# Kernel tuning notes

Measured on AMD Instinct MI355X. Metric: run time of the kernel, lower is better.

The kernel has to match this reference:

```python
import jax, jax.numpy as jnp
import numpy as np

N_NODES = 100000
N_EDGES = 1600000
D_IN = 256
N_HEADS = 4
D_OUT = 32
NEG_SLOPE = 0.2


def setup_inputs() -> dict:
    key = jax.random.key(0)
    k1, k2, k3, k4, k5, k6 = jax.random.split(key, 6)
    x = jax.random.normal(k1, (N_NODES, D_IN), dtype=jnp.float32)
    fc_w = jax.random.normal(k2, (N_HEADS * D_OUT, D_IN), dtype=jnp.float32) * (1.0 / np.sqrt(D_IN))
    attn_l = jax.random.normal(k3, (N_HEADS, D_OUT), dtype=jnp.float32) * 0.1
    attn_r = jax.random.normal(k4, (N_HEADS, D_OUT), dtype=jnp.float32) * 0.1
    src = jax.random.randint(k5, (N_EDGES,), 0, N_NODES, dtype=jnp.int64)
    dst = jax.random.randint(k6, (N_EDGES,), 0, N_NODES, dtype=jnp.int64)
    return {"x": x, "fc_w": fc_w, "attn_l": attn_l, "attn_r": attn_r, "src": src, "dst": dst}


def reference(x, fc_w, attn_l, attn_r, src, dst):
    N = x.shape[0]
    H, F = attn_l.shape
    # Linear projection: ft = fc(x) viewed as [N, H, F]
    ft = (x @ fc_w.T).reshape(N, H, F)
    # Per-node attention logits: el = <ft, a_l>, er = <ft, a_r>  -> [N, H]
    el = jnp.einsum("nhf,hf->nh", ft, attn_l)
    er = jnp.einsum("nhf,hf->nh", ft, attn_r)
    # Edge scores: e = leaky_relu(el[src] + er[dst])  -> [E, H]
    e = el[src] + er[dst]
    e = jnp.where(e > 0, e, NEG_SLOPE * e)
    # Segment (per-destination-node) softmax over incoming edges
    m = jax.ops.segment_max(e, dst, num_segments=N)  # [N, H]
    ex = jnp.exp(e - m[dst])                          # [E, H]
    denom = jax.ops.segment_sum(ex, dst, num_segments=N)  # [N, H]
    a = ex / denom[dst]                               # [E, H]
    # Weighted scatter-sum aggregation: out[n] = sum_{e: dst=n} a_e * ft[src_e]
    out = jax.ops.segment_sum(ft[src] * a[:, :, None], dst, num_segments=N)  # [N, H, F]
    return out
```

## Files before the change

### kernel.cpp

```cpp
#include <hip/hip_runtime.h>
#include <math.h>

#define N_NODES 100000
#define N_EDGES 1600000
#define D_IN 256
#define N_HEADS 4
#define D_OUT 32
#define D_HID 128
#define NEG_SLOPE 0.2f

#define BUCKET_SHIFT 8
#define BUCKET_NODES 256
#define NB ((N_NODES + BUCKET_NODES - 1) / BUCKET_NODES)
#define CAP 6144
#define TILE 8192
#define N_TILES ((N_EDGES + TILE - 1) / TILE)

typedef __attribute__((ext_vector_type(8))) short bf16x8;
typedef __attribute__((ext_vector_type(4))) float f32x4;

static __device__ __forceinline__ unsigned short f2bf(float f) {
  union { float f; unsigned u; } c; c.f = f;
  unsigned r = c.u + 0x7FFFu + ((c.u >> 16) & 1u);
  return (unsigned short)(r >> 16);
}
static __device__ __forceinline__ float bfu_lo(unsigned u) {
  union { unsigned u; float f; } c; c.u = u << 16; return c.f;
}
static __device__ __forceinline__ float bfu_hi(unsigned u) {
  union { unsigned u; float f; } c; c.u = u & 0xFFFF0000u; return c.f;
}

#define LDA 40
__global__ __launch_bounds__(256) void k_gemm(const float* __restrict__ x,
                                              const float* __restrict__ w,
                                              unsigned short* __restrict__ ftb) {
  __shared__ short As[128 * LDA];
  __shared__ short Bs[128 * LDA];
  int t = threadIdx.x;
  int wave = t >> 6, lane = t & 63;
  int quad = lane >> 4, l16 = lane & 15;
  int rowBase = blockIdx.x * 128;
  int wm = (wave >> 1) * 64, wn = (wave & 1) * 64;
  f32x4 acc[4][4];
  #pragma unroll
  for (int mt = 0; mt < 4; ++mt)
    #pragma unroll
    for (int nt = 0; nt < 4; ++nt) {
      acc[mt][nt][0] = 0.f; acc[mt][nt][1] = 0.f;
      acc[mt][nt][2] = 0.f; acc[mt][nt][3] = 0.f;
    }

  for (int kb = 0; kb < D_IN; kb += 32) {
    #pragma unroll
    for (int p = 0; p < 4; ++p) {
      int idx = p * 256 + t;
      int r = idx >> 3;
      int kq = (idx & 7) * 4;
      int row = rowBase + r;
      float4 v = make_float4(0.f, 0.f, 0.f, 0.f);
      if (row < N_NODES) v = *(const float4*)&x[(size_t)row * D_IN + kb + kq];
      short* d = &As[r * LDA + kq];
      d[0] = (short)f2bf(v.x); d[1] = (short)f2bf(v.y);
      d[2] = (short)f2bf(v.z); d[3] = (short)f2bf(v.w);
    }
    #pragma unroll
    for (int p = 0; p < 4; ++p) {
      int idx = p * 256 + t;
      int r = idx >> 3;
      int kq = (idx & 7) * 4;
      float4 v = *(const float4*)&w[(size_t)r * D_IN + kb + kq];
      short* d = &Bs[r * LDA + kq];
      d[0] = (short)f2bf(v.x); d[1] = (short)f2bf(v.y);
      d[2] = (short)f2bf(v.z); d[3] = (short)f2bf(v.w);
    }
    __syncthreads();
    bf16x8 af[4], bfr[4];
    #pragma unroll
    for (int mt = 0; mt < 4; ++mt)
      af[mt] = *(const bf16x8*)&As[(wm + mt * 16 + l16) * LDA + quad * 8];
    #pragma unroll
    for (int nt = 0; nt < 4; ++nt)
      bfr[nt] = *(const bf16x8*)&Bs[(wn + nt * 16 + l16) * LDA + quad * 8];
    #pragma unroll
    for (int mt = 0; mt < 4; ++mt)
      #pragma unroll
      for (int nt = 0; nt < 4; ++nt)
        acc[mt][nt] = __builtin_amdgcn_mfma_f32_16x16x32_bf16(af[mt], bfr[nt], acc[mt][nt], 0, 0, 0);
    __syncthreads();
  }
  #pragma unroll
  for (int mt = 0; mt < 4; ++mt) {
    #pragma unroll
    for (int nt = 0; nt < 4; ++nt) {
      int col = wn + nt * 16 + l16;
      #pragma unroll
      for (int r = 0; r < 4; ++r) {
        int row = rowBase + wm + mt * 16 + quad * 4 + r;
        if (row < N_NODES)
          ftb[(size_t)row * D_HID + col] = f2bf(acc[mt][nt][r]);
      }
    }
  }
}

__global__ void k_eler(const unsigned short* __restrict__ ftb,
                       const float* __restrict__ al,
                       const float* __restrict__ ar,
                       float* __restrict__ el, float* __restrict__ er) {
  int gid = blockIdx.x * blockDim.x + threadIdx.x;
  if (gid >= N_NODES * N_HEADS) return;
  int n = gid >> 2, h = gid & 3;
  const unsigned* f = (const unsigned*)&ftb[(size_t)n * D_HID + h * D_OUT];
  const float* alh = &al[h * D_OUT];
  const float* arh = &ar[h * D_OUT];
  float sl = 0.f, sr = 0.f;
  #pragma unroll
  for (int i = 0; i < 16; ++i) {
    unsigned u = f[i];
    float lo = bfu_lo(u), hi = bfu_hi(u);
    sl += lo * alh[2 * i] + hi * alh[2 * i + 1];
    sr += lo * arh[2 * i] + hi * arh[2 * i + 1];
  }
  el[gid] = sl;
  er[gid] = sr;
}

__global__ __launch_bounds__(256) void k_bucket(const int* __restrict__ src,
                                                const int* __restrict__ dst,
                                                int* __restrict__ gfill,
                                                unsigned* __restrict__ pairs) {
  __shared__ int bcnt[NB];
  __shared__ int brsv[NB];
  __shared__ int brank[NB];
  int t = threadIdx.x;
  for (int tile = blockIdx.x; tile < N_TILES; tile += gridDim.x) {
    int e0 = tile * TILE;
    int e1 = min(e0 + TILE, N_EDGES);
    for (int i = t; i < NB; i += 256) { bcnt[i] = 0; brank[i] = 0; }
    __syncthreads();
    for (int i = e0 + t; i < e1; i += 256)
      atomicAdd(&bcnt[dst[i] >> BUCKET_SHIFT], 1);
    __syncthreads();
    for (int i = t; i < NB; i += 256) {
      int c = bcnt[i];
      brsv[i] = (c > 0) ? atomicAdd(&gfill[i], c) : 0;
    }
    __syncthreads();
    for (int i = e0 + t; i < e1; i += 256) {
      int d = dst[i];
      int s = src[i];
      int b = d >> BUCKET_SHIFT;
      int r = brsv[b] + atomicAdd(&brank[b], 1);
      if (r < CAP)
        pairs[(size_t)b * CAP + r] = ((unsigned)s << 8) | (unsigned)(d & (BUCKET_NODES - 1));
    }
    __syncthreads();
  }
}

__global__ __launch_bounds__(512) void k_scanbuckets(const int* __restrict__ gfill,
                                                     int* __restrict__ bbase,
                                                     int* __restrict__ offs) {
  __shared__ int ss[512];
  int t = threadIdx.x;
  int v = (t < NB) ? gfill[t] : 0;
  ss[t] = v;
  __syncthreads();
  #pragma unroll
  for (int d = 1; d < 512; d <<= 1) {
    int u = (t >= d) ? ss[t - d] : 0;
    __syncthreads();
    ss[t] += u;
    __syncthreads();
  }
  if (t < NB) bbase[t] = (t == 0) ? 0 : ss[t - 1];
  if (t == 0) offs[N_NODES] = N_EDGES;
}

__global__ __launch_bounds__(256) void k_localsort(const unsigned* __restrict__ pairs,
                                                   const int* __restrict__ gfill,
                                                   const int* __restrict__ bbase,
                                                   int* __restrict__ offs,
                                                   int* __restrict__ ssrc) {
  __shared__ int cnt_l[256];
  __shared__ int ss[256];
  __shared__ int cur_l[256];
  int b = blockIdx.x, t = threadIdx.x;
  int E = min(gfill[b], CAP);
  int base = bbase[b];
  const unsigned* pb = &pairs[(size_t)b * CAP];
  cnt_l[t] = 0;
  __syncthreads();
  for (int i = t; i < E; i += 256)
    atomicAdd(&cnt_l[pb[i] & (BUCKET_NODES - 1)], 1);
  __syncthreads();
  int v = cnt_l[t];
  ss[t] = v;
  __syncthreads();
  #pragma unroll
  for (int d = 1; d < 256; d <<= 1) {
    int u = (t >= d) ? ss[t - d] : 0;
    __syncthreads();
    ss[t] += u;
    __syncthreads();
  }
  int pre = (t == 0) ? 0 : ss[t - 1];
  int node = b * BUCKET_NODES + t;
  if (node < N_NODES) offs[node] = base + pre;
  cur_l[t] = pre;
  __syncthreads();
  for (int i = t; i < E; i += 256) {
    unsigned p = pb[i];
    int pos = atomicAdd(&cur_l[p & (BUCKET_NODES - 1)], 1);
    ssrc[base + pos] = (int)(p >> 8);
  }
}

__global__ __launch_bounds__(256) void k_agg(const int* __restrict__ offs,
                                             const int* __restrict__ ssrc,
                                             const unsigned short* __restrict__ ftb,
                                             const float* __restrict__ el,
                                             const float* __restrict__ er,
                                             float* __restrict__ out) {
  __shared__ int   lds_s[4][64];
  __shared__ float lds_a[4][64][4];
  int wave = threadIdx.x >> 6;
  int lane = threadIdx.x & 63;
  int n = blockIdx.x * 4 + wave;
  if (n >= N_NODES) return;
  int start = offs[n], end = offs[n + 1];
  int deg = end - start;
  int f0 = lane * 2;
  int hh = lane >> 4;
  float2 acc = {0.f, 0.f};

  if (deg > 0 && deg <= 64) {
    float4 er4 = *(const float4*)&er[n * 4];
    bool valid = lane < deg;
    int s = valid ? ssrc[start + lane] : 0;
    float4 e4 = *(const float4*)&el[s * 4];
    float v[4] = {e4.x + er4.x, e4.y + er4.y, e4.z + er4.z, e4.w + er4.w};
    float m[4], ex[4], den[4];
    #pragma unroll
    for (int h = 0; h < 4; ++h) {
      v[h] = v[h] > 0.f ? v[h] : NEG_SLOPE * v[h];
      m[h] = valid ? v[h] : -INFINITY;
    }
    #pragma unroll
    for (int h = 0; h < 4; ++h)
      #pragma unroll
      for (int o = 32; o > 0; o >>= 1) m[h] = fmaxf(m[h], __shfl_xor(m[h], o));
    #pragma unroll
    for (int h = 0; h < 4; ++h) {
      ex[h] = valid ? __expf(v[h] - m[h]) : 0.f;
      den[h] = ex[h];
    }
    #pragma unroll
    for (int h = 0; h < 4; ++h)
      #pragma unroll
      for (int o = 32; o > 0; o >>= 1) den[h] += __shfl_xor(den[h], o);
    float4 a4 = make_float4(ex[0] / den[0], ex[1] / den[1], ex[2] / den[2], ex[3] / den[3]);
    lds_s[wave][lane] = s;
    *(float4*)&lds_a[wave][lane][0] = a4;
    __builtin_amdgcn_wave_barrier();
    for (int j = 0; j < deg; ++j) {
      int sj = lds_s[wave][j];
      float a = lds_a[wave][j][hh];
      unsigned u = *(const unsigned*)&ftb[(size_t)sj * D_HID + f0];
      acc.x += a * bfu_lo(u);
      acc.y += a * bfu_hi(u);
    }
  } else if (deg > 64) {
    float4 er4 = *(const float4*)&er[n * 4];
    float erh[4] = {er4.x, er4.y, er4.z, er4.w};
    float m[4] = {-INFINITY, -INFINITY, -INFINITY, -INFINITY};
    for (int c = start; c < end; c += 64) {
      int i = c + lane;
      bool valid = i < end;
      int s = valid ? ssrc[i] : 0;
      float4 e4 = *(const float4*)&el[s * 4];
      float ee[4] = {e4.x, e4.y, e4.z, e4.w};
      #pragma unroll
      for (int h = 0; h < 4; ++h) {
        float v = ee[h] + erh[h];
        v = v > 0.f ? v : NEG_SLOPE * v;
        if (!valid) v = -INFINITY;
        m[h] = fmaxf(m[h], v);
      }
    }
    #pragma unroll
    for (int h = 0; h < 4; ++h)
      #pragma unroll
      for (int o = 32; o > 0; o >>= 1) m[h] = fmaxf(m[h], __shfl_xor(m[h], o));
    float den[4] = {0.f, 0.f, 0.f, 0.f};
    for (int c = start; c < end; c += 64) {
      int i = c + lane;
      bool valid = i < end;
      int s = valid ? ssrc[i] : 0;
      float4 e4 = *(const float4*)&el[s * 4];
      float ee[4] = {e4.x, e4.y, e4.z, e4.w};
      #pragma unroll
      for (int h = 0; h < 4; ++h) {
        float v = ee[h] + erh[h];
        v = v > 0.f ? v : NEG_SLOPE * v;
        den[h] += valid ? __expf(v - m[h]) : 0.f;
      }
    }
    #pragma unroll
    for (int h = 0; h < 4; ++h)
      #pragma unroll
      for (int o = 32; o > 0; o >>= 1) den[h] += __shfl_xor(den[h], o);
    float invd = 1.f / den[hh];
    for (int c = start; c < end; c += 64) {
      int i = c + lane;
      bool valid = i < end;
      int s = valid ? ssrc[i] : 0;
      float4 e4 = *(const float4*)&el[s * 4];
      float ee[4] = {e4.x, e4.y, e4.z, e4.w};
      float ex[4];
      #pragma unroll
      for (int h = 0; h < 4; ++h) {
        float v = ee[h] + erh[h];
        v = v > 0.f ? v : NEG_SLOPE * v;
        ex[h] = __expf(v - m[h]);
      }
      int cnt2 = min(64, end - c);
      for (int j = 0; j < cnt2; ++j) {
        int sj = __shfl(s, j);
        float a0 = __shfl(ex[0], j);
        float a1 = __shfl(ex[1], j);
        float a2 = __shfl(ex[2], j);
        float a3 = __shfl(ex[3], j);
        float ah = hh == 0 ? a0 : (hh == 1 ? a1 : (hh == 2 ? a2 : a3));
        ah *= invd;
        unsigned u = *(const unsigned*)&ftb[(size_t)sj * D_HID + f0];
        acc.x += ah * bfu_lo(u);
        acc.y += ah * bfu_hi(u);
      }
    }
  }
  *(float2*)&out[(size_t)n * D_HID + f0] = acc;
}

extern "C" void kernel_launch(void* const* d_in, const int* in_sizes, int n_in,
                              void* d_out, int out_size, void* d_ws, size_t ws_size,
                              hipStream_t stream) {
  const float* x      = (const float*)d_in[0];
  const float* fc_w   = (const float*)d_in[1];
  const float* attn_l = (const float*)d_in[2];
  const float* attn_r = (const float*)d_in[3];
  const int*   src    = (const int*)d_in[4];
  const int*   dst    = (const int*)d_in[5];
  float* out = (float*)d_out;

  char* wsp = (char*)d_ws;
  size_t off = 0;
  auto alloc = [&](size_t bytes) {
    void* p = wsp + off;
    off = (off + bytes + 255) & ~(size_t)255;
    return p;
  };
  unsigned short* ftb = (unsigned short*)alloc((size_t)N_NODES * D_HID * 2);
  float* el     = (float*)alloc((size_t)N_NODES * 4 * 4);
  float* er     = (float*)alloc((size_t)N_NODES * 4 * 4);
  int*   offs   = (int*)alloc((size_t)(N_NODES + 1) * 4);
  int*   ssrc   = (int*)alloc((size_t)N_EDGES * 4);
  int*   gfill  = (int*)alloc((size_t)NB * 4);
  int*   bbase  = (int*)alloc((size_t)NB * 4);
  unsigned* pairs = (unsigned*)alloc((size_t)NB * CAP * 4);

  hipMemsetAsync(gfill, 0, (size_t)NB * 4, stream);
  k_gemm<<<(N_NODES + 127) / 128, 256, 0, stream>>>(x, fc_w, ftb);
  k_eler<<<(N_NODES * N_HEADS + 255) / 256, 256, 0, stream>>>(ftb, attn_l, attn_r, el, er);
  k_bucket<<<N_TILES, 256, 0, stream>>>(src, dst, gfill, pairs);
  k_scanbuckets<<<1, 512, 0, stream>>>(gfill, bbase, offs);
  k_localsort<<<NB, 256, 0, stream>>>(pairs, gfill, bbase, offs, ssrc);
  k_agg<<<(N_NODES + 3) / 4, 256, 0, stream>>>(offs, ssrc, ftb, el, er, out);
}
```

Baseline: 359.3 us.

## Vectorize aggregation gathers across four edges and use packed bf16 conversion

The low-degree path of the aggregation kernel now has each quarter-wave handle a different edge, loading 16-byte feature chunks per lane and then reducing across quarters with shuffles. The aim is more memory-level parallelism and fewer, wider gather loads. The GEMM replaces the software bf16 rounding with the packed v_cvt_pk_bf16_f32 instruction. The local sort runs with 512 threads per block and the bucketing tile size shrinks. The cost is an extra cross-lane reduction and idle threads during the local-sort scan.

```diff
diff --git a/kernel.cpp b/kernel.cpp
--- a/kernel.cpp
+++ b/kernel.cpp
@@ -13,16 +13,17 @@
 #define BUCKET_NODES 256
 #define NB ((N_NODES + BUCKET_NODES - 1) / BUCKET_NODES)
 #define CAP 6144
-#define TILE 8192
+#define TILE 2048
 #define N_TILES ((N_EDGES + TILE - 1) / TILE)
 
 typedef __attribute__((ext_vector_type(8))) short bf16x8;
 typedef __attribute__((ext_vector_type(4))) float f32x4;
-
-static __device__ __forceinline__ unsigned short f2bf(float f) {
-  union { float f; unsigned u; } c; c.f = f;
-  unsigned r = c.u + 0x7FFFu + ((c.u >> 16) & 1u);
-  return (unsigned short)(r >> 16);
+typedef __attribute__((ext_vector_type(4))) unsigned int u32x4;
+
+static __device__ __forceinline__ unsigned cvt2(float lo, float hi) {
+  unsigned r;
+  asm("v_cvt_pk_bf16_f32 %0, %1, %2" : "=v"(r) : "v"(lo), "v"(hi));
+  return r;
 }
 static __device__ __forceinline__ float bfu_lo(unsigned u) {
   union { unsigned u; float f; } c; c.u = u << 16; return c.f;
@@ -60,9 +61,9 @@
       int row = rowBase + r;
       float4 v = make_float4(0.f, 0.f, 0.f, 0.f);
       if (row < N_NODES) v = *(const float4*)&x[(size_t)row * D_IN + kb + kq];
-      short* d = &As[r * LDA + kq];
-      d[0] = (short)f2bf(v.x); d[1] = (short)f2bf(v.y);
-      d[2] = (short)f2bf(v.z); d[3] = (short)f2bf(v.w);
+      unsigned* d = (unsigned*)&As[r * LDA + kq];
+      d[0] = cvt2(v.x, v.y);
+      d[1] = cvt2(v.z, v.w);
     }
     #pragma unroll
     for (int p = 0; p < 4; ++p) {
@@ -70,9 +71,9 @@
       int r = idx >> 3;
       int kq = (idx & 7) * 4;
       float4 v = *(const float4*)&w[(size_t)r * D_IN + kb + kq];
-      short* d = &Bs[r * LDA + kq];
-      d[0] = (short)f2bf(v.x); d[1] = (short)f2bf(v.y);
-      d[2] = (short)f2bf(v.z); d[3] = (short)f2bf(v.w);
+      unsigned* d = (unsigned*)&Bs[r * LDA + kq];
+      d[0] = cvt2(v.x, v.y);
+      d[1] = cvt2(v.z, v.w);
     }
     __syncthreads();
     bf16x8 af[4], bfr[4];
@@ -95,10 +96,13 @@
     for (int nt = 0; nt < 4; ++nt) {
       int col = wn + nt * 16 + l16;
       #pragma unroll
-      for (int r = 0; r < 4; ++r) {
+      for (int r = 0; r < 4; r += 2) {
+        unsigned p = cvt2(acc[mt][nt][r], acc[mt][nt][r + 1]);
         int row = rowBase + wm + mt * 16 + quad * 4 + r;
         if (row < N_NODES)
-          ftb[(size_t)row * D_HID + col] = f2bf(acc[mt][nt][r]);
+          ftb[(size_t)row * D_HID + col] = (unsigned short)p;
+        if (row + 1 < N_NODES)
+          ftb[(size_t)(row + 1) * D_HID + col] = (unsigned short)(p >> 16);
       }
     }
   }
@@ -178,7 +182,7 @@
   if (t == 0) offs[N_NODES] = N_EDGES;
 }
 
-__global__ __launch_bounds__(256) void k_localsort(const unsigned* __restrict__ pairs,
+__global__ __launch_bounds__(512) void k_localsort(const unsigned* __restrict__ pairs,
                                                    const int* __restrict__ gfill,
                                                    const int* __restrict__ bbase,
                                                    int* __restrict__ offs,
@@ -190,27 +194,28 @@
   int E = min(gfill[b], CAP);
   int base = bbase[b];
   const unsigned* pb = &pairs[(size_t)b * CAP];
-  cnt_l[t] = 0;
+  if (t < 256) cnt_l[t] = 0;
   __syncthreads();
-  for (int i = t; i < E; i += 256)
+  for (int i = t; i < E; i += 512)
     atomicAdd(&cnt_l[pb[i] & (BUCKET_NODES - 1)], 1);
   __syncthreads();
-  int v = cnt_l[t];
-  ss[t] = v;
+  if (t < 256) ss[t] = cnt_l[t];
   __syncthreads();
   #pragma unroll
   for (int d = 1; d < 256; d <<= 1) {
-    int u = (t >= d) ? ss[t - d] : 0;
-    __syncthreads();
-    ss[t] += u;
-    __syncthreads();
-  }
-  int pre = (t == 0) ? 0 : ss[t - 1];
-  int node = b * BUCKET_NODES + t;
-  if (node < N_NODES) offs[node] = base + pre;
-  cur_l[t] = pre;
+    int u = (t < 256 && t >= d) ? ss[t - d] : 0;
+    __syncthreads();
+    if (t < 256) ss[t] += u;
+    __syncthreads();
+  }
+  if (t < 256) {
+    int pre = (t == 0) ? 0 : ss[t - 1];
+    int node = b * BUCKET_NODES + t;
+    if (node < N_NODES) offs[node] = base + pre;
+    cur_l[t] = pre;
+  }
   __syncthreads();
-  for (int i = t; i < E; i += 256) {
+  for (int i = t; i < E; i += 512) {
     unsigned p = pb[i];
     int pos = atomicAdd(&cur_l[p & (BUCKET_NODES - 1)], 1);
     ssrc[base + pos] = (int)(p >> 8);
@@ -231,11 +236,8 @@
   if (n >= N_NODES) return;
   int start = offs[n], end = offs[n + 1];
   int deg = end - start;
-  int f0 = lane * 2;
-  int hh = lane >> 4;
-  float2 acc = {0.f, 0.f};
-
-  if (deg > 0 && deg <= 64) {
+
+  if (deg <= 64) {
     float4 er4 = *(const float4*)&er[n * 4];
     bool valid = lane < deg;
     int s = valid ? ssrc[start + lane] : 0;
@@ -264,14 +266,35 @@
     lds_s[wave][lane] = s;
     *(float4*)&lds_a[wave][lane][0] = a4;
     __builtin_amdgcn_wave_barrier();
-    for (int j = 0; j < deg; ++j) {
-      int sj = lds_s[wave][j];
-      float a = lds_a[wave][j][hh];
-      unsigned u = *(const unsigned*)&ftb[(size_t)sj * D_HID + f0];
-      acc.x += a * bfu_lo(u);
-      acc.y += a * bfu_hi(u);
-    }
-  } else if (deg > 64) {
+    int quad = lane >> 4, l4 = lane & 15;
+    int head = l4 >> 2;
+    const unsigned short* fb = ftb + l4 * 8;
+    float acc[8] = {0.f, 0.f, 0.f, 0.f, 0.f, 0.f, 0.f, 0.f};
+    for (int j = 0; j < deg; j += 4) {
+      int e = j + quad;
+      int sj = lds_s[wave][e];
+      float a = lds_a[wave][e][head];
+      u32x4 u = *(const u32x4*)&fb[(size_t)sj * D_HID];
+      acc[0] += a * bfu_lo(u.x); acc[1] += a * bfu_hi(u.x);
+      acc[2] += a * bfu_lo(u.y); acc[3] += a * bfu_hi(u.y);
+      acc[4] += a * bfu_lo(u.z); acc[5] += a * bfu_hi(u.z);
+      acc[6] += a * bfu_lo(u.w); acc[7] += a * bfu_hi(u.w);
+    }
+    #pragma unroll
+    for (int i = 0; i < 8; ++i) {
+      acc[i] += __shfl_xor(acc[i], 16);
+      acc[i] += __shfl_xor(acc[i], 32);
+    }
+    if (quad == 0) {
+      float4 o0 = make_float4(acc[0], acc[1], acc[2], acc[3]);
+      float4 o1 = make_float4(acc[4], acc[5], acc[6], acc[7]);
+      *(float4*)&out[(size_t)n * D_HID + l4 * 8] = o0;
+      *(float4*)&out[(size_t)n * D_HID + l4 * 8 + 4] = o1;
+    }
+  } else {
+    int f0 = lane * 2;
+    int hh = lane >> 4;
+    float2 acc = {0.f, 0.f};
     float4 er4 = *(const float4*)&er[n * 4];
     float erh[4] = {er4.x, er4.y, er4.z, er4.w};
     float m[4] = {-INFINITY, -INFINITY, -INFINITY, -INFINITY};
@@ -339,8 +362,8 @@
         acc.y += ah * bfu_hi(u);
       }
     }
-  }
-  *(float2*)&out[(size_t)n * D_HID + f0] = acc;
+    *(float2*)&out[(size_t)n * D_HID + f0] = acc;
+  }
 }
 
 extern "C" void kernel_launch(void* const* d_in, const int* in_sizes, int n_in,
@@ -375,6 +398,6 @@
   k_eler<<<(N_NODES * N_HEADS + 255) / 256, 256, 0, stream>>>(ftb, attn_l, attn_r, el, er);
   k_bucket<<<N_TILES, 256, 0, stream>>>(src, dst, gfill, pairs);
   k_scanbuckets<<<1, 512, 0, stream>>>(gfill, bbase, offs);
-  k_localsort<<<NB, 256, 0, stream>>>(pairs, gfill, bbase, offs, ssrc);
+  k_localsort<<<NB, 512, 0, stream>>>(pairs, gfill, bbase, offs, ssrc);
   k_agg<<<(N_NODES + 3) / 4, 256, 0, stream>>>(offs, ssrc, ftb, el, er, out);
 }
```

Result: faster. 344.3 us (-4.2%).
